# Performance work log

Measured on AMD Instinct MI355X. Metric: run time of the kernel, lower is better.

## Reference

```python
import jax, jax.numpy as jnp
import numpy as np

N = 100000
E = 3200000
IN_DIM = 256
OUT_DIM = 256
BN_EPS = 1e-5


def setup_inputs() -> dict:
    key = jax.random.key(0)
    k1, k2, k3, k4, k5 = jax.random.split(key, 5)
    x = jax.random.normal(k1, (N, IN_DIM), dtype=jnp.float32)
    edge_rows = jax.random.randint(k2, (E,), 0, N, dtype=jnp.int32)
    edge_cols = jax.random.randint(k3, (E,), 0, N, dtype=jnp.int32)
    edge_vals = jax.random.uniform(k4, (E,), dtype=jnp.float32)
    # xavier_uniform-like init for weight
    limit = float(np.sqrt(6.0 / (IN_DIM + OUT_DIM)))
    weight = jax.random.uniform(k5, (IN_DIM, OUT_DIM), minval=-limit, maxval=limit, dtype=jnp.float32)
    gamma = jnp.ones((OUT_DIM,), dtype=jnp.float32)
    beta = jnp.zeros((OUT_DIM,), dtype=jnp.float32)
    return {"x": x, "edge_rows": edge_rows, "edge_cols": edge_cols,
            "edge_vals": edge_vals, "weight": weight, "gamma": gamma, "beta": beta}


def reference(x, edge_rows, edge_cols, edge_vals, weight, gamma, beta):
    # dense projection: [N, in] @ [in, out] -> [N, out]
    z = jnp.matmul(x, weight)
    # sparse adjacency matmul (spmm): gather source rows, scale, scatter-add to dest
    msgs = edge_vals[:, None] * z[edge_cols]          # [E, out]
    agg = jax.ops.segment_sum(msgs, edge_rows, num_segments=N)  # [N, out]
    # BatchNorm1d (training mode: batch stats, biased variance) + ReLU
    mean = jnp.mean(agg, axis=0)
    var = jnp.mean(jnp.square(agg - mean), axis=0)
    norm = (agg - mean) * jax.lax.rsqrt(var + BN_EPS) * gamma + beta
    return jax.nn.relu(norm)
```

## Files before the change

kernel.cpp:

```cpp
#include <hip/hip_runtime.h>
#include <hip/hip_bf16.h>

#define N_NODES 100000
#define N_EDGES 3200000
#define DIM 256
#define BN_EPS 1e-5f
#define BROWS 256
#define NBUCK ((N_NODES + BROWS - 1) / BROWS)
#define BIN_BLOCKS 512
#define EPB (N_EDGES / BIN_BLOCKS)

typedef __attribute__((ext_vector_type(8))) short short8v;
typedef __attribute__((ext_vector_type(4))) float f32x4;

__device__ __forceinline__ float b2f(unsigned short h) {
    return __uint_as_float(((unsigned int)h) << 16);
}
__device__ __forceinline__ unsigned short f2b(float f) {
    unsigned int u = __float_as_uint(f);
    unsigned int rounded = u + 0x7FFF + ((u >> 16) & 1);
    return (unsigned short)(rounded >> 16);
}

__global__ __launch_bounds__(256) void wfrag_kernel(const float* __restrict__ W,
                                                    unsigned short* __restrict__ wfrag) {
    const int t = blockIdx.x * 256 + threadIdx.x;
    const int e = t & 7;
    const int l = (t >> 3) & 63;
    const int frag = t >> 9;
    const int nt = frag >> 3;
    const int ks = frag & 7;
    const int k = ks * 32 + ((l >> 4) << 3) + e;
    const int c = nt * 16 + (l & 15);
    wfrag[t] = f2b(W[k * DIM + c]);
}

__global__ __launch_bounds__(256) void gemm_mfma_kernel(const float* __restrict__ x,
                                                        const unsigned short* __restrict__ wfrag,
                                                        unsigned short* __restrict__ zb) {
    const int wid = (blockIdx.x * blockDim.x + threadIdx.x) >> 6;
    const int lane = threadIdx.x & 63;
    if (wid >= N_NODES / 16) return;
    const int m0 = wid * 16;

    const int arow = m0 + (lane & 15);
    const int kb = (lane >> 4) << 3;
    const float* xrow = x + (size_t)arow * DIM + kb;
    short8v af[8];
    #pragma unroll
    for (int ks = 0; ks < 8; ++ks) {
        const float4 a0 = *(const float4*)(xrow + ks * 32);
        const float4 a1 = *(const float4*)(xrow + ks * 32 + 4);
        short8v f;
        f[0] = (short)f2b(a0.x); f[1] = (short)f2b(a0.y);
        f[2] = (short)f2b(a0.z); f[3] = (short)f2b(a0.w);
        f[4] = (short)f2b(a1.x); f[5] = (short)f2b(a1.y);
        f[6] = (short)f2b(a1.z); f[7] = (short)f2b(a1.w);
        af[ks] = f;
    }

    const int drow0 = m0 + ((lane >> 4) << 2);
    const int dcol = lane & 15;
    for (int nt = 0; nt < 16; ++nt) {
        f32x4 acc = {0.f, 0.f, 0.f, 0.f};
        const unsigned short* wp = wfrag + ((size_t)(nt * 8) * 64 + lane) * 8;
        #pragma unroll
        for (int ks = 0; ks < 8; ++ks) {
            const short8v bf = *(const short8v*)(wp + (size_t)ks * 64 * 8);
            acc = __builtin_amdgcn_mfma_f32_16x16x32_bf16(af[ks], bf, acc, 0, 0, 0);
        }
        unsigned short* zp = zb + (size_t)drow0 * DIM + nt * 16 + dcol;
        zp[0]       = f2b(acc[0]);
        zp[DIM]     = f2b(acc[1]);
        zp[2 * DIM] = f2b(acc[2]);
        zp[3 * DIM] = f2b(acc[3]);
    }
}

__global__ __launch_bounds__(256) void coarse_hist_kernel(const int* __restrict__ rows,
                                                          int* __restrict__ coarse) {
    __shared__ int h[NBUCK];
    const int t = threadIdx.x;
    for (int i = t; i < NBUCK; i += 256) h[i] = 0;
    __syncthreads();
    const int stride = gridDim.x * 256;
    for (int e = blockIdx.x * 256 + t; e < N_EDGES; e += stride)
        atomicAdd(&h[rows[e] >> 8], 1);
    __syncthreads();
    for (int i = t; i < NBUCK; i += 256)
        if (h[i]) atomicAdd(&coarse[i], h[i]);
}

__global__ __launch_bounds__(512) void scan_coarse_kernel(const int* __restrict__ coarse,
                                                          int* __restrict__ coarseBase,
                                                          int* __restrict__ gCursor,
                                                          int* __restrict__ row_ptr) {
    __shared__ int s[512];
    const int t = threadIdx.x;
    const int v = (t < NBUCK) ? coarse[t] : 0;
    s[t] = v;
    __syncthreads();
    for (int off = 1; off < 512; off <<= 1) {
        int x = (t >= off) ? s[t - off] : 0;
        __syncthreads();
        s[t] += x;
        __syncthreads();
    }
    if (t < NBUCK) {
        coarseBase[t] = s[t] - v;
        gCursor[t] = s[t] - v;
    }
    if (t == 0) row_ptr[N_NODES] = N_EDGES;
}

__global__ __launch_bounds__(256) void bin_kernel(const int* __restrict__ rows,
                                                  const int* __restrict__ cols,
                                                  const float* __restrict__ vals,
                                                  int* gCursor,
                                                  int2* __restrict__ gBinned) {
    __shared__ int h[NBUCK];
    __shared__ int base[NBUCK];
    __shared__ int cur[NBUCK];
    const int t = threadIdx.x;
    const int e0 = blockIdx.x * EPB;
    for (int i = t; i < NBUCK; i += 256) h[i] = 0;
    __syncthreads();
    for (int e = e0 + t; e < e0 + EPB; e += 256)
        atomicAdd(&h[rows[e] >> 8], 1);
    __syncthreads();
    for (int b = t; b < NBUCK; b += 256) {
        cur[b] = 0;
        if (h[b]) base[b] = atomicAdd(&gCursor[b], h[b]);
    }
    __syncthreads();
    for (int e = e0 + t; e < e0 + EPB; e += 256) {
        const int r = rows[e];
        const int b = r >> 8;
        const int rk = atomicAdd(&cur[b], 1);
        int2 p;
        p.x = ((r & 255) << 17) | cols[e];
        p.y = __float_as_int(vals[e]);
        gBinned[base[b] + rk] = p;
    }
}

__global__ __launch_bounds__(256) void fine_sort_kernel(const int* __restrict__ coarse,
                                                        const int* __restrict__ coarseBase,
                                                        const int2* __restrict__ gBinned,
                                                        int* __restrict__ row_ptr,
                                                        int2* __restrict__ finalE) {
    __shared__ int h[BROWS];
    __shared__ int s[BROWS];
    __shared__ int cur[BROWS];
    const int t = threadIdx.x;
    const int b = blockIdx.x;
    const int base0 = coarseBase[b];
    const int cnt = coarse[b];
    h[t] = 0;
    __syncthreads();
    for (int e = base0 + t; e < base0 + cnt; e += 256)
        atomicAdd(&h[gBinned[e].x >> 17], 1);
    __syncthreads();
    s[t] = h[t];
    __syncthreads();
    for (int off = 1; off < BROWS; off <<= 1) {
        int x = (t >= off) ? s[t - off] : 0;
        __syncthreads();
        s[t] += x;
        __syncthreads();
    }
    const int excl = s[t] - h[t];
    const int grow = b * BROWS + t;
    if (grow < N_NODES) row_ptr[grow] = base0 + excl;
    cur[t] = excl;
    __syncthreads();
    for (int e = base0 + t; e < base0 + cnt; e += 256) {
        const int2 p = gBinned[e];
        const int rl = p.x >> 17;
        const int rk = atomicAdd(&cur[rl], 1);
        int2 q;
        q.x = p.x & 0x1FFFF;
        q.y = p.y;
        finalE[base0 + rk] = q;
    }
}

__global__ __launch_bounds__(256) void spmm_csr_kernel(const int* __restrict__ row_ptr,
                                                       const int2* __restrict__ pairs,
                                                       const unsigned short* __restrict__ zb,
                                                       float* __restrict__ out) {
    const int wave = (blockIdx.x * blockDim.x + threadIdx.x) >> 6;
    const int lane = threadIdx.x & 63;
    if (wave >= N_NODES) return;
    const int start = row_ptr[wave];
    const int end = row_ptr[wave + 1];
    float4 acc = make_float4(0.f, 0.f, 0.f, 0.f);
    int e = start;
    for (; e + 3 < end; e += 4) {
        const int2 p0 = pairs[e],     p1 = pairs[e + 1];
        const int2 p2 = pairs[e + 2], p3 = pairs[e + 3];
        const float v0 = __int_as_float(p0.y), v1 = __int_as_float(p1.y);
        const float v2 = __int_as_float(p2.y), v3 = __int_as_float(p3.y);
        const ushort4 m0 = ((const ushort4*)(zb + (size_t)p0.x * DIM))[lane];
        const ushort4 m1 = ((const ushort4*)(zb + (size_t)p1.x * DIM))[lane];
        const ushort4 m2 = ((const ushort4*)(zb + (size_t)p2.x * DIM))[lane];
        const ushort4 m3 = ((const ushort4*)(zb + (size_t)p3.x * DIM))[lane];
        acc.x += v0 * b2f(m0.x) + v1 * b2f(m1.x) + v2 * b2f(m2.x) + v3 * b2f(m3.x);
        acc.y += v0 * b2f(m0.y) + v1 * b2f(m1.y) + v2 * b2f(m2.y) + v3 * b2f(m3.y);
        acc.z += v0 * b2f(m0.z) + v1 * b2f(m1.z) + v2 * b2f(m2.z) + v3 * b2f(m3.z);
        acc.w += v0 * b2f(m0.w) + v1 * b2f(m1.w) + v2 * b2f(m2.w) + v3 * b2f(m3.w);
    }
    for (; e < end; ++e) {
        const int2 p0 = pairs[e];
        const float v0 = __int_as_float(p0.y);
        const ushort4 m0 = ((const ushort4*)(zb + (size_t)p0.x * DIM))[lane];
        acc.x += v0 * b2f(m0.x);
        acc.y += v0 * b2f(m0.y);
        acc.z += v0 * b2f(m0.z);
        acc.w += v0 * b2f(m0.w);
    }
    ((float4*)(out + (size_t)wave * DIM))[lane] = acc;
}

#define STATS_ROWS 128
__global__ __launch_bounds__(256) void stats_kernel(const float* __restrict__ agg,
                                                    float* __restrict__ stats) {
    const int c = threadIdx.x;
    const int row0 = blockIdx.x * STATS_ROWS;
    const int row1 = min(row0 + STATS_ROWS, N_NODES);
    float s = 0.f, ss = 0.f;
    for (int r = row0; r < row1; ++r) {
        float a = agg[(size_t)r * DIM + c];
        s += a;
        ss += a * a;
    }
    atomicAdd(&stats[c], s);
    atomicAdd(&stats[DIM + c], ss);
}

__global__ __launch_bounds__(256) void finalize_kernel(const float* __restrict__ stats,
                                                       const float* __restrict__ gamma,
                                                       const float* __restrict__ beta,
                                                       float* __restrict__ sb) {
    const int c = threadIdx.x;
    const float inv_n = 1.0f / (float)N_NODES;
    const float mean = stats[c] * inv_n;
    float var = stats[DIM + c] * inv_n - mean * mean;
    const float rstd = rsqrtf(var + BN_EPS);
    const float scale = rstd * gamma[c];
    sb[c] = scale;
    sb[DIM + c] = beta[c] - mean * scale;
}

__global__ __launch_bounds__(256) void norm_kernel(float* __restrict__ out,
                                                   const float* __restrict__ sb) {
    const int nvec = N_NODES * (DIM / 4);
    const int stride = gridDim.x * blockDim.x;
    for (int idx = blockIdx.x * blockDim.x + threadIdx.x; idx < nvec; idx += stride) {
        const int c0 = (idx & 63) * 4;
        float4 a = ((float4*)out)[idx];
        float4 o;
        o.x = fmaxf(fmaf(a.x, sb[c0 + 0], sb[DIM + c0 + 0]), 0.f);
        o.y = fmaxf(fmaf(a.y, sb[c0 + 1], sb[DIM + c0 + 1]), 0.f);
        o.z = fmaxf(fmaf(a.z, sb[c0 + 2], sb[DIM + c0 + 2]), 0.f);
        o.w = fmaxf(fmaf(a.w, sb[c0 + 3], sb[DIM + c0 + 3]), 0.f);
        ((float4*)out)[idx] = o;
    }
}

extern "C" void kernel_launch(void* const* d_in, const int* in_sizes, int n_in,
                              void* d_out, int out_size, void* d_ws, size_t ws_size,
                              hipStream_t stream) {
    const float* x         = (const float*)d_in[0];
    const int*   edge_rows = (const int*)d_in[1];
    const int*   edge_cols = (const int*)d_in[2];
    const float* edge_vals = (const float*)d_in[3];
    const float* weight    = (const float*)d_in[4];
    const float* gamma     = (const float*)d_in[5];
    const float* beta      = (const float*)d_in[6];
    float* out = (float*)d_out;

    unsigned short* zb    = (unsigned short*)d_ws;
    unsigned short* wfrag = zb + (size_t)N_NODES * DIM;
    int2*  gBinned  = (int2*)(wfrag + DIM * DIM);
    int2*  finalE   = gBinned + N_EDGES;
    int*   row_ptr  = (int*)(finalE + N_EDGES);
    int*   coarse   = row_ptr + N_NODES + 1;
    float* stats    = (float*)(coarse + 392);
    float* sb       = stats + 2 * DIM;
    int*   coarseBase = (int*)(sb + 2 * DIM);
    int*   gCursor  = coarseBase + 392;

    hipMemsetAsync(coarse, 0, (392 + 512) * sizeof(int), stream);

    wfrag_kernel<<<DIM * DIM / 256, 256, 0, stream>>>(weight, wfrag);
    gemm_mfma_kernel<<<(N_NODES / 16 + 3) / 4, 256, 0, stream>>>(x, wfrag, zb);

    coarse_hist_kernel<<<BIN_BLOCKS, 256, 0, stream>>>(edge_rows, coarse);
    scan_coarse_kernel<<<1, 512, 0, stream>>>(coarse, coarseBase, gCursor, row_ptr);
    bin_kernel<<<BIN_BLOCKS, 256, 0, stream>>>(edge_rows, edge_cols, edge_vals, gCursor, gBinned);
    fine_sort_kernel<<<NBUCK, 256, 0, stream>>>(coarse, coarseBase, gBinned, row_ptr, finalE);

    spmm_csr_kernel<<<(N_NODES * 64 + 255) / 256, 256, 0, stream>>>(row_ptr, finalE, zb, out);

    stats_kernel<<<(N_NODES + STATS_ROWS - 1) / STATS_ROWS, 256, 0, stream>>>(out, stats);
    finalize_kernel<<<1, 256, 0, stream>>>(stats, gamma, beta, sb);
    norm_kernel<<<2048, 256, 0, stream>>>(out, sb);
}
```

Measured before the change: 527.0 us.

## Fuse BatchNorm statistics into SpMM epilogue with partitioned partial sums

The SpMM kernel now processes four rows per wave and accumulates per-channel sum and sum of squares in registers, reduces them in shared memory, and atomically adds the results into 64 partitioned global buffers. This removes the separate stats pass that re-read the whole aggregated output. The gather loop is also unrolled to eight edges with wave-uniform row bounds, and norm_kernel hoists its scale and bias loads out of the loop. In exchange, each wave does more sequential work, and the grid size assumes N_NODES is divisible by 16.

```diff
diff --git a/kernel.cpp b/kernel.cpp
--- a/kernel.cpp
+++ b/kernel.cpp
@@ -9,6 +9,8 @@
 #define NBUCK ((N_NODES + BROWS - 1) / BROWS)
 #define BIN_BLOCKS 512
 #define EPB (N_EDGES / BIN_BLOCKS)
+#define RPW 4
+#define NPART 64
 
 typedef __attribute__((ext_vector_type(8))) short short8v;
 typedef __attribute__((ext_vector_type(4))) float f32x4;
@@ -188,82 +190,108 @@
 __global__ __launch_bounds__(256) void spmm_csr_kernel(const int* __restrict__ row_ptr,
                                                        const int2* __restrict__ pairs,
                                                        const unsigned short* __restrict__ zb,
-                                                       float* __restrict__ out) {
-    const int wave = (blockIdx.x * blockDim.x + threadIdx.x) >> 6;
-    const int lane = threadIdx.x & 63;
-    if (wave >= N_NODES) return;
-    const int start = row_ptr[wave];
-    const int end = row_ptr[wave + 1];
-    float4 acc = make_float4(0.f, 0.f, 0.f, 0.f);
-    int e = start;
-    for (; e + 3 < end; e += 4) {
-        const int2 p0 = pairs[e],     p1 = pairs[e + 1];
-        const int2 p2 = pairs[e + 2], p3 = pairs[e + 3];
-        const float v0 = __int_as_float(p0.y), v1 = __int_as_float(p1.y);
-        const float v2 = __int_as_float(p2.y), v3 = __int_as_float(p3.y);
-        const ushort4 m0 = ((const ushort4*)(zb + (size_t)p0.x * DIM))[lane];
-        const ushort4 m1 = ((const ushort4*)(zb + (size_t)p1.x * DIM))[lane];
-        const ushort4 m2 = ((const ushort4*)(zb + (size_t)p2.x * DIM))[lane];
-        const ushort4 m3 = ((const ushort4*)(zb + (size_t)p3.x * DIM))[lane];
-        acc.x += v0 * b2f(m0.x) + v1 * b2f(m1.x) + v2 * b2f(m2.x) + v3 * b2f(m3.x);
-        acc.y += v0 * b2f(m0.y) + v1 * b2f(m1.y) + v2 * b2f(m2.y) + v3 * b2f(m3.y);
-        acc.z += v0 * b2f(m0.z) + v1 * b2f(m1.z) + v2 * b2f(m2.z) + v3 * b2f(m3.z);
-        acc.w += v0 * b2f(m0.w) + v1 * b2f(m1.w) + v2 * b2f(m2.w) + v3 * b2f(m3.w);
-    }
-    for (; e < end; ++e) {
-        const int2 p0 = pairs[e];
-        const float v0 = __int_as_float(p0.y);
-        const ushort4 m0 = ((const ushort4*)(zb + (size_t)p0.x * DIM))[lane];
-        acc.x += v0 * b2f(m0.x);
-        acc.y += v0 * b2f(m0.y);
-        acc.z += v0 * b2f(m0.z);
-        acc.w += v0 * b2f(m0.w);
-    }
-    ((float4*)(out + (size_t)wave * DIM))[lane] = acc;
-}
-
-#define STATS_ROWS 128
-__global__ __launch_bounds__(256) void stats_kernel(const float* __restrict__ agg,
-                                                    float* __restrict__ stats) {
-    const int c = threadIdx.x;
-    const int row0 = blockIdx.x * STATS_ROWS;
-    const int row1 = min(row0 + STATS_ROWS, N_NODES);
-    float s = 0.f, ss = 0.f;
-    for (int r = row0; r < row1; ++r) {
-        float a = agg[(size_t)r * DIM + c];
-        s += a;
-        ss += a * a;
-    }
-    atomicAdd(&stats[c], s);
-    atomicAdd(&stats[DIM + c], ss);
-}
-
-__global__ __launch_bounds__(256) void finalize_kernel(const float* __restrict__ stats,
+                                                       float* __restrict__ out,
+                                                       float* __restrict__ partials) {
+    __shared__ float sdata[2 * DIM];
+    const int t = threadIdx.x;
+    sdata[t] = 0.f;
+    sdata[t + 256] = 0.f;
+    __syncthreads();
+
+    const int wave = (blockIdx.x * 256 + t) >> 6;
+    const int lane = t & 63;
+    const int row0 = wave * RPW;
+
+    float4 s  = make_float4(0.f, 0.f, 0.f, 0.f);
+    float4 sq = make_float4(0.f, 0.f, 0.f, 0.f);
+
+    for (int row = row0; row < row0 + RPW; ++row) {
+        const int start = __builtin_amdgcn_readfirstlane(row_ptr[row]);
+        const int end   = __builtin_amdgcn_readfirstlane(row_ptr[row + 1]);
+        float4 acc = make_float4(0.f, 0.f, 0.f, 0.f);
+        int e = start;
+        for (; e + 8 <= end; e += 8) {
+            int2 p[8];
+            #pragma unroll
+            for (int j = 0; j < 8; ++j) p[j] = pairs[e + j];
+            ushort4 m[8];
+            #pragma unroll
+            for (int j = 0; j < 8; ++j)
+                m[j] = ((const ushort4*)(zb + (size_t)p[j].x * DIM))[lane];
+            #pragma unroll
+            for (int j = 0; j < 8; ++j) {
+                const float v = __int_as_float(p[j].y);
+                acc.x += v * b2f(m[j].x);
+                acc.y += v * b2f(m[j].y);
+                acc.z += v * b2f(m[j].z);
+                acc.w += v * b2f(m[j].w);
+            }
+        }
+        for (; e < end; ++e) {
+            const int2 p0 = pairs[e];
+            const float v0 = __int_as_float(p0.y);
+            const ushort4 m0 = ((const ushort4*)(zb + (size_t)p0.x * DIM))[lane];
+            acc.x += v0 * b2f(m0.x);
+            acc.y += v0 * b2f(m0.y);
+            acc.z += v0 * b2f(m0.z);
+            acc.w += v0 * b2f(m0.w);
+        }
+        ((float4*)(out + (size_t)row * DIM))[lane] = acc;
+        s.x += acc.x; s.y += acc.y; s.z += acc.z; s.w += acc.w;
+        sq.x += acc.x * acc.x; sq.y += acc.y * acc.y;
+        sq.z += acc.z * acc.z; sq.w += acc.w * acc.w;
+    }
+
+    const int c0 = lane * 4;
+    atomicAdd(&sdata[c0 + 0], s.x);
+    atomicAdd(&sdata[c0 + 1], s.y);
+    atomicAdd(&sdata[c0 + 2], s.z);
+    atomicAdd(&sdata[c0 + 3], s.w);
+    atomicAdd(&sdata[256 + c0 + 0], sq.x);
+    atomicAdd(&sdata[256 + c0 + 1], sq.y);
+    atomicAdd(&sdata[256 + c0 + 2], sq.z);
+    atomicAdd(&sdata[256 + c0 + 3], sq.w);
+    __syncthreads();
+
+    float* pb = partials + (size_t)(blockIdx.x & (NPART - 1)) * (2 * DIM);
+    atomicAdd(&pb[t], sdata[t]);
+    atomicAdd(&pb[t + 256], sdata[t + 256]);
+}
+
+__global__ __launch_bounds__(256) void finalize_kernel(const float* __restrict__ partials,
                                                        const float* __restrict__ gamma,
                                                        const float* __restrict__ beta,
                                                        float* __restrict__ sb) {
     const int c = threadIdx.x;
+    float s = 0.f, ssq = 0.f;
+    for (int b = 0; b < NPART; ++b) {
+        s   += partials[b * (2 * DIM) + c];
+        ssq += partials[b * (2 * DIM) + 256 + c];
+    }
     const float inv_n = 1.0f / (float)N_NODES;
-    const float mean = stats[c] * inv_n;
-    float var = stats[DIM + c] * inv_n - mean * mean;
+    const float mean = s * inv_n;
+    float var = ssq * inv_n - mean * mean;
     const float rstd = rsqrtf(var + BN_EPS);
     const float scale = rstd * gamma[c];
     sb[c] = scale;
     sb[DIM + c] = beta[c] - mean * scale;
 }
 
+#define NORM_BLOCKS 2048
 __global__ __launch_bounds__(256) void norm_kernel(float* __restrict__ out,
                                                    const float* __restrict__ sb) {
+    const int c0 = (threadIdx.x & 63) * 4;
+    const float s0 = sb[c0 + 0], s1 = sb[c0 + 1], s2 = sb[c0 + 2], s3 = sb[c0 + 3];
+    const float b0 = sb[DIM + c0 + 0], b1 = sb[DIM + c0 + 1];
+    const float b2 = sb[DIM + c0 + 2], b3 = sb[DIM + c0 + 3];
     const int nvec = N_NODES * (DIM / 4);
-    const int stride = gridDim.x * blockDim.x;
-    for (int idx = blockIdx.x * blockDim.x + threadIdx.x; idx < nvec; idx += stride) {
-        const int c0 = (idx & 63) * 4;
+    for (int idx = blockIdx.x * 256 + threadIdx.x; idx < nvec; idx += NORM_BLOCKS * 256) {
         float4 a = ((float4*)out)[idx];
         float4 o;
-        o.x = fmaxf(fmaf(a.x, sb[c0 + 0], sb[DIM + c0 + 0]), 0.f);
-        o.y = fmaxf(fmaf(a.y, sb[c0 + 1], sb[DIM + c0 + 1]), 0.f);
-        o.z = fmaxf(fmaf(a.z, sb[c0 + 2], sb[DIM + c0 + 2]), 0.f);
-        o.w = fmaxf(fmaf(a.w, sb[c0 + 3], sb[DIM + c0 + 3]), 0.f);
+        o.x = fmaxf(fmaf(a.x, s0, b0), 0.f);
+        o.y = fmaxf(fmaf(a.y, s1, b1), 0.f);
+        o.z = fmaxf(fmaf(a.z, s2, b2), 0.f);
+        o.w = fmaxf(fmaf(a.w, s3, b3), 0.f);
         ((float4*)out)[idx] = o;
     }
 }
@@ -286,12 +314,12 @@
     int2*  finalE   = gBinned + N_EDGES;
     int*   row_ptr  = (int*)(finalE + N_EDGES);
     int*   coarse   = row_ptr + N_NODES + 1;
-    float* stats    = (float*)(coarse + 392);
-    float* sb       = stats + 2 * DIM;
+    float* partials = (float*)(coarse + 392);
+    float* sb       = partials + NPART * 2 * DIM;
     int*   coarseBase = (int*)(sb + 2 * DIM);
     int*   gCursor  = coarseBase + 392;
 
-    hipMemsetAsync(coarse, 0, (392 + 512) * sizeof(int), stream);
+    hipMemsetAsync(coarse, 0, (392 + NPART * 2 * DIM) * sizeof(int), stream);
 
     wfrag_kernel<<<DIM * DIM / 256, 256, 0, stream>>>(weight, wfrag);
     gemm_mfma_kernel<<<(N_NODES / 16 + 3) / 4, 256, 0, stream>>>(x, wfrag, zb);
@@ -301,9 +329,8 @@
     bin_kernel<<<BIN_BLOCKS, 256, 0, stream>>>(edge_rows, edge_cols, edge_vals, gCursor, gBinned);
     fine_sort_kernel<<<NBUCK, 256, 0, stream>>>(coarse, coarseBase, gBinned, row_ptr, finalE);
 
-    spmm_csr_kernel<<<(N_NODES * 64 + 255) / 256, 256, 0, stream>>>(row_ptr, finalE, zb, out);
-
-    stats_kernel<<<(N_NODES + STATS_ROWS - 1) / STATS_ROWS, 256, 0, stream>>>(out, stats);
-    finalize_kernel<<<1, 256, 0, stream>>>(stats, gamma, beta, sb);
-    norm_kernel<<<2048, 256, 0, stream>>>(out, sb);
-}
+    spmm_csr_kernel<<<N_NODES / (RPW * 4), 256, 0, stream>>>(row_ptr, finalE, zb, out, partials);
+
+    finalize_kernel<<<1, 256, 0, stream>>>(partials, gamma, beta, sb);
+    norm_kernel<<<NORM_BLOCKS, 256, 0, stream>>>(out, sb);
+}
```

New measurement: 487.0 us. -7.6%, faster.
